# Performance work log

Hardware: AMD Instinct MI355X
Metric: run time of the kernel (lower is better)

## Reference

```python
import jax, jax.numpy as jnp
import numpy as np
import math

DIM = 1024
MLP = 4096
D_STATE = 16
D_CONV = 4
EXPAND = 2
D_INNER = EXPAND * DIM
HALF = D_INNER // 2
DT_RANK = math.ceil(DIM / 16)
BSZ = 2
SEQ = 2048
LN_EPS = 1e-5


def setup_inputs() -> dict:
    key = jax.random.key(0)
    ks = jax.random.split(key, 12)
    s = lambda k, shape, sc: jax.random.normal(k, shape, dtype=jnp.float32) * sc
    return {
        "x": s(ks[0], (BSZ, SEQ, DIM), 1.0),
        "ln1_g": jnp.ones((DIM,), jnp.float32),
        "ln1_b": jnp.zeros((DIM,), jnp.float32),
        "in_proj_w": s(ks[1], (D_INNER, DIM), 0.02),
        "conv_x_w": s(ks[2], (HALF, 1, D_CONV), 0.1),
        "conv_x_b": jnp.zeros((HALF,), jnp.float32),
        "conv_z_w": s(ks[3], (HALF, 1, D_CONV), 0.1),
        "conv_z_b": jnp.zeros((HALF,), jnp.float32),
        "x_proj_w": s(ks[4], (DT_RANK + 2 * D_STATE, HALF), 0.02),
        "dt_proj_w": s(ks[5], (HALF, DT_RANK), 0.02),
        "dt_proj_b": s(ks[6], (HALF,), 0.1),
        "A_log": jnp.log(jnp.tile(jnp.arange(1, D_STATE + 1, dtype=jnp.float32), (HALF, 1))),
        "Dp": jnp.ones((HALF,), jnp.float32),
        "out_proj_w": s(ks[7], (DIM, D_INNER), 0.02),
        "ln2_g": jnp.ones((DIM,), jnp.float32),
        "ln2_b": jnp.zeros((DIM,), jnp.float32),
        "mlp_w1": s(ks[8], (MLP, DIM), 0.02),
        "mlp_b1": jnp.zeros((MLP,), jnp.float32),
        "mlp_w2": s(ks[9], (DIM, MLP), 0.02),
        "mlp_b2": jnp.zeros((DIM,), jnp.float32),
    }


def _ln(x, g, b):
    mu = jnp.mean(x, -1, keepdims=True)
    v = jnp.mean((x - mu) ** 2, -1, keepdims=True)
    return (x - mu) * jax.lax.rsqrt(v + LN_EPS) * g + b


def _dwconv_same(x, w, b):
    # x: [B, C, L]; w: [C, 1, K] depthwise; PyTorch 'same' pads left=(K-1)//2, right=rest
    total = D_CONV - 1
    left = total // 2
    y = jax.lax.conv_general_dilated(
        x, w, (1,), [(left, total - left)],
        dimension_numbers=("NCH", "OIH", "NCH"),
        feature_group_count=x.shape[1])
    return y + b[None, :, None]


def _mixer(x, in_proj_w, conv_x_w, conv_x_b, conv_z_w, conv_z_b,
           x_proj_w, dt_proj_w, dt_proj_b, A_log, Dp, out_proj_w):
    Bsz = x.shape[0]
    xz = jnp.einsum('bld,ed->ble', x, in_proj_w)              # [B,L,2*HALF]
    xs, zs = jnp.split(xz, 2, axis=-1)
    xc = jax.nn.silu(_dwconv_same(jnp.swapaxes(xs, 1, 2), conv_x_w, conv_x_b))  # [B,HALF,L]
    zc = jax.nn.silu(_dwconv_same(jnp.swapaxes(zs, 1, 2), conv_z_w, conv_z_b))  # [B,HALF,L]
    u = jnp.swapaxes(xc, 1, 2)                                 # [B,L,HALF]
    x_dbl = jnp.einsum('bld,ed->ble', u, x_proj_w)             # [B,L,dt_rank+2N]
    dt, Bm, Cm = jnp.split(x_dbl, [DT_RANK, DT_RANK + D_STATE], axis=-1)
    delta = jax.nn.softplus(jnp.einsum('blr,dr->bld', dt, dt_proj_w) + dt_proj_b)  # [B,L,HALF]
    A = -jnp.exp(A_log)                                        # [HALF,N]
    dA = jnp.exp(jnp.einsum('bld,dn->lbdn', delta, A))         # [L,B,HALF,N]
    dBu = jnp.einsum('bld,bln,bld->lbdn', delta, Bm, u)        # [L,B,HALF,N]
    Cs = jnp.moveaxis(Cm, 1, 0)                                # [L,B,N]

    def step(h, t):
        dA_t, dBu_t, c_t = t
        h = dA_t * h + dBu_t                                   # [B,HALF,N]
        return h, jnp.einsum('bdn,bn->bd', h, c_t)

    h0 = jnp.zeros((Bsz, HALF, D_STATE), x.dtype)
    _, ys = jax.lax.scan(step, h0, (dA, dBu, Cs))              # ys: [L,B,HALF]
    y = jnp.moveaxis(ys, 0, 1) + u * Dp                        # [B,L,HALF]
    y = jnp.concatenate([y, jnp.swapaxes(zc, 1, 2)], axis=-1)  # [B,L,2*HALF]
    return jnp.einsum('ble,de->bld', y, out_proj_w)


def reference(x, ln1_g, ln1_b, in_proj_w, conv_x_w, conv_x_b, conv_z_w, conv_z_b,
              x_proj_w, dt_proj_w, dt_proj_b, A_log, Dp, out_proj_w,
              ln2_g, ln2_b, mlp_w1, mlp_b1, mlp_w2, mlp_b2):
    x = x + _mixer(_ln(x, ln1_g, ln1_b), in_proj_w, conv_x_w, conv_x_b,
                   conv_z_w, conv_z_b, x_proj_w, dt_proj_w, dt_proj_b,
                   A_log, Dp, out_proj_w)
    h = _ln(x, ln2_g, ln2_b)
    h = jax.nn.gelu(jnp.einsum('bld,md->blm', h, mlp_w1) + mlp_b1, approximate=False)
    h = jnp.einsum('blm,dm->bld', h, mlp_w2) + mlp_b2
    return x + h
```

## Files before the change

### kernel.cpp

```cpp
#include <hip/hip_runtime.h>
#include <math.h>

#define DIMD    1024
#define MLPD    4096
#define DSTATE  16
#define DCONV   4
#define HALF    1024
#define DINNER  2048
#define DTRANK  64
#define BSZ     2
#define SEQ     2048
#define NTOK    (BSZ*SEQ)
#define NCH     64
#define CL      (SEQ/NCH)

typedef short bf16x8 __attribute__((ext_vector_type(8)));
typedef float f32x4  __attribute__((ext_vector_type(4)));
typedef float f32x16 __attribute__((ext_vector_type(16)));
typedef unsigned short u16;
typedef unsigned int   u32;
typedef unsigned short u16x4 __attribute__((ext_vector_type(4)));

__device__ __forceinline__ u16 f2bf(float x) {
    union { float f; unsigned int u; } v; v.f = x;
    unsigned int r = (v.u + 0x7FFFu + ((v.u >> 16) & 1u)) >> 16;
    return (u16)r;
}
__device__ __forceinline__ float bf2f(u16 x) {
    union { unsigned int u; float f; } v; v.u = ((unsigned int)x) << 16;
    return v.f;
}

#define SZ_WIN  (DINNER*DIMD)
#define SZ_WXP  (96*HALF)
#define SZ_WDT  (HALF*DTRANK)
#define SZ_WOUT (DIMD*DINNER)
#define SZ_WM1  (MLPD*DIMD)
#define SZ_WM2  (DIMD*MLPD)
#define SZ_TOT  (SZ_WIN+SZ_WXP+SZ_WDT+SZ_WOUT+SZ_WM1+SZ_WM2)
#define CVT_BLOCKS (SZ_TOT / 1024)

__global__ __launch_bounds__(256) void cvtln_kernel(
        const float* __restrict__ x, const float* __restrict__ g,
        const float* __restrict__ b, u16* __restrict__ xn_bf,
        const float* __restrict__ s0, u16* __restrict__ d0,
        const float* __restrict__ s1, u16* __restrict__ d1,
        const float* __restrict__ s2, u16* __restrict__ d2,
        const float* __restrict__ s3, u16* __restrict__ d3,
        const float* __restrict__ s4, u16* __restrict__ d4,
        const float* __restrict__ s5, u16* __restrict__ d5) {
    if (blockIdx.x >= NTOK) {
        int i = (blockIdx.x - NTOK) * 1024 + threadIdx.x * 4;
        #define CVT4(s, d) { \
            float4 v = *(const float4*)((s) + i); \
            u16x4 o; o[0]=f2bf(v.x); o[1]=f2bf(v.y); o[2]=f2bf(v.z); o[3]=f2bf(v.w); \
            *(u16x4*)((d) + i) = o; }
        if (i < SZ_WIN)  { CVT4(s0, d0); return; }  i -= SZ_WIN;
        if (i < SZ_WXP)  { CVT4(s1, d1); return; }  i -= SZ_WXP;
        if (i < SZ_WDT)  { CVT4(s2, d2); return; }  i -= SZ_WDT;
        if (i < SZ_WOUT) { CVT4(s3, d3); return; }  i -= SZ_WOUT;
        if (i < SZ_WM1)  { CVT4(s4, d4); return; }  i -= SZ_WM1;
        if (i < SZ_WM2)  { CVT4(s5, d5); }
        #undef CVT4
        return;
    }
    __shared__ float sm[4];
    int row = blockIdx.x;
    int t = threadIdx.x;
    const float4* xr = (const float4*)(x + (size_t)row * DIMD);
    float4 v = xr[t];
    float s = v.x + v.y + v.z + v.w;
    for (int off = 32; off > 0; off >>= 1) s += __shfl_down(s, off, 64);
    if ((t & 63) == 0) sm[t >> 6] = s;
    __syncthreads();
    float mu = (sm[0] + sm[1] + sm[2] + sm[3]) * (1.0f / DIMD);
    float dx = v.x - mu, dy = v.y - mu, dz = v.z - mu, dw = v.w - mu;
    float ss = dx*dx + dy*dy + dz*dz + dw*dw;
    for (int off = 32; off > 0; off >>= 1) ss += __shfl_down(ss, off, 64);
    __syncthreads();
    if ((t & 63) == 0) sm[t >> 6] = ss;
    __syncthreads();
    float var = (sm[0] + sm[1] + sm[2] + sm[3]) * (1.0f / DIMD);
    float rs = rsqrtf(var + 1e-5f);
    float4 gv = ((const float4*)g)[t];
    float4 bv = ((const float4*)b)[t];
    u16* o = xn_bf + (size_t)row * DIMD + t * 4;
    o[0] = f2bf(dx * rs * gv.x + bv.x);
    o[1] = f2bf(dy * rs * gv.y + bv.y);
    o[2] = f2bf(dz * rs * gv.z + bv.z);
    o[3] = f2bf(dw * rs * gv.w + bv.w);
}

__global__ __launch_bounds__(256) void gemm_small_kernel(
        const u16* __restrict__ A, int lda,
        const u16* __restrict__ W, int K, int N,
        float* __restrict__ Cf, u16* __restrict__ Cb) {
    __shared__ f32x4 red[2][64];
    int t = threadIdx.x;
    int w = t >> 6, lane = t & 63;
    int mt = w & 1, kh = w >> 1;
    int m0 = blockIdx.x * 32 + mt * 16;
    int n0 = blockIdx.y * 16;
    int r = lane & 15, quad = lane >> 4;
    int Kh = K >> 1;
    f32x4 acc = {0.f, 0.f, 0.f, 0.f};
    const u16* ap = A + (size_t)(m0 + r) * lda + kh * Kh + quad * 8;
    const u16* wp = W + (size_t)(n0 + r) * K   + kh * Kh + quad * 8;
    for (int k = 0; k < Kh; k += 32) {
        bf16x8 av = *(const bf16x8*)(ap + k);
        bf16x8 bv = *(const bf16x8*)(wp + k);
        acc = __builtin_amdgcn_mfma_f32_16x16x32_bf16(av, bv, acc, 0, 0, 0);
    }
    if (kh == 1) red[mt][lane] = acc;
    __syncthreads();
    if (kh == 0) {
        f32x4 o = red[mt][lane];
        int col = n0 + r;
        #pragma unroll
        for (int i = 0; i < 4; ++i) {
            int row = m0 + quad * 4 + i;
            size_t idx = (size_t)row * N + col;
            float v = acc[i] + o[i];
            Cf[idx] = v;
            Cb[idx] = f2bf(v);
        }
    }
}

template<int EPI, int TN, int KS>
__global__ __launch_bounds__(256) void gemm128_kernel(
        const u16* __restrict__ A, int lda, const u16* __restrict__ W,
        int K, int N,
        const float* __restrict__ bias, const float* __restrict__ resid,
        float* __restrict__ Cf, float* __restrict__ Cf2,
        float* __restrict__ Cf3, float* __restrict__ Cf4,
        u16* __restrict__ Cb) {
    constexpr int NF = TN / 32;
    constexpr int NN = TN / 64;
    __shared__ u16 As0[128 * 32], As1[128 * 32];
    __shared__ u16 Bs0[TN * 32],  Bs1[TN * 32];
    const int t = threadIdx.x;
    const int w = t >> 6;
    const int lane = t & 63;
    const int r32 = lane & 31;
    const int kh  = lane >> 5;
    const int wm = w & 1, wn = w >> 1;
    const int m0 = blockIdx.x * 128;
    const int n0 = blockIdx.y * TN;
    const int Kloc = K / KS;
    const int kz = (KS > 1) ? blockIdx.z : 0;

    f32x16 acc[2][NN];
    #pragma unroll
    for (int mi = 0; mi < 2; ++mi)
        #pragma unroll
        for (int ni = 0; ni < NN; ++ni)
            acc[mi][ni] = (f32x16){0.f,0.f,0.f,0.f,0.f,0.f,0.f,0.f,
                                   0.f,0.f,0.f,0.f,0.f,0.f,0.f,0.f};

    const u16* pa[2];
    const u16* pb[NF / 2];
    #pragma unroll
    for (int i = 0; i < 2; ++i) {
        int c = (i * 4 + w) * 64 + lane;
        int row = c >> 2;
        int q = (c & 3) ^ ((row >> 1) & 3);
        pa[i] = A + (size_t)(m0 + row) * lda + (size_t)kz * Kloc + q * 8;
    }
    #pragma unroll
    for (int i = 0; i < NF / 2; ++i) {
        int c = (i * 4 + w) * 64 + lane;
        int row = c >> 2;
        int q = (c & 3) ^ ((row >> 1) & 3);
        pb[i] = W + (size_t)(n0 + row) * K + (size_t)kz * Kloc + q * 8;
    }
    const int gsw = (r32 >> 1) & 3;
    int aoff[2][2], boff[NN][2];
    #pragma unroll
    for (int mi = 0; mi < 2; ++mi)
        #pragma unroll
        for (int tt = 0; tt < 2; ++tt)
            aoff[mi][tt] = (wm * 64 + mi * 32 + r32) * 32 +
                           ((tt * 2 + kh) ^ gsw) * 8;
    #pragma unroll
    for (int ni = 0; ni < NN; ++ni)
        #pragma unroll
        for (int tt = 0; tt < 2; ++tt)
            boff[ni][tt] = (wn * (TN / 2) + ni * 32 + r32) * 32 +
                           ((tt * 2 + kh) ^ gsw) * 8;

    auto stage = [&](u16* __restrict__ Ad, u16* __restrict__ Bd) {
        #pragma unroll
        for (int i = 0; i < 2; ++i) {
            __builtin_amdgcn_global_load_lds(
                (const __attribute__((address_space(1))) u32*)pa[i],
                (__attribute__((address_space(3))) u32*)(Ad + (i * 4 + w) * 512),
                16, 0, 0);
            pa[i] += 32;
        }
        #pragma unroll
        for (int i = 0; i < NF / 2; ++i) {
            __builtin_amdgcn_global_load_lds(
                (const __attribute__((address_space(1))) u32*)pb[i],
                (__attribute__((address_space(3))) u32*)(Bd + (i * 4 + w) * 512),
                16, 0, 0);
            pb[i] += 32;
        }
    };
    auto compute = [&](const u16* __restrict__ Ab, const u16* __restrict__ Bb) {
        bf16x8 af[2][2], bfr[NN][2];
        #pragma unroll
        for (int mi = 0; mi < 2; ++mi)
            #pragma unroll
            for (int tt = 0; tt < 2; ++tt)
                af[mi][tt] = *(const bf16x8*)(Ab + aoff[mi][tt]);
        #pragma unroll
        for (int ni = 0; ni < NN; ++ni)
            #pragma unroll
            for (int tt = 0; tt < 2; ++tt)
                bfr[ni][tt] = *(const bf16x8*)(Bb + boff[ni][tt]);
        #pragma unroll
        for (int tt = 0; tt < 2; ++tt)
            #pragma unroll
            for (int mi = 0; mi < 2; ++mi)
                #pragma unroll
                for (int ni = 0; ni < NN; ++ni)
                    acc[mi][ni] = __builtin_amdgcn_mfma_f32_32x32x16_bf16(
                        af[mi][tt], bfr[ni][tt], acc[mi][ni], 0, 0, 0);
    };

    stage(As0, Bs0);
    for (int k0 = 0; k0 < Kloc; k0 += 64) {
        __syncthreads();
        if (k0 + 32 < Kloc) stage(As1, Bs1);
        compute(As0, Bs0);
        __syncthreads();
        if (k0 + 64 < Kloc) stage(As0, Bs0);
        compute(As1, Bs1);
    }

    float* Cfo = Cf;
    if (KS == 2 && kz == 1) Cfo = Cf2;
    if (KS == 4) Cfo = (kz == 0) ? Cf : (kz == 1) ? Cf2 : (kz == 2) ? Cf3 : Cf4;
    #pragma unroll
    for (int mi = 0; mi < 2; ++mi) {
        #pragma unroll
        for (int ni = 0; ni < NN; ++ni) {
            #pragma unroll
            for (int reg = 0; reg < 16; ++reg) {
                int row = m0 + wm * 64 + mi * 32 + (reg & 3) + 8 * (reg >> 2) + 4 * kh;
                int col = n0 + wn * (TN / 2) + ni * 32 + r32;
                size_t idx = (size_t)row * N + col;
                float v = acc[mi][ni][reg];
                if (EPI == 1) { v += bias[col]; v = (v > 20.f) ? v : log1pf(expf(v)); }
                if (EPI == 2) {
                    v += bias[col];
                    float e = __expf(fminf(1.5957691216f * v + 0.0713548162f * v * v * v, 80.f));
                    v = v * __fdividef(e, e + 1.f);
                }
                if (EPI == 3) { v += resid[idx]; }
                if (EPI == 4) { v += bias[col] + resid[idx]; }
                if (EPI == 2 || EPI == 5) Cb[idx] = f2bf(v);
                else                      Cfo[idx] = v;
            }
        }
    }
}

template<int EPI, int KS_>
__global__ __launch_bounds__(512) void gemm256_kernel(
        const u16* __restrict__ A, int lda, const u16* __restrict__ W,
        int K, int N,
        const float* __restrict__ bias,
        float* __restrict__ Cf, float* __restrict__ Cf2,
        float* __restrict__ Cf3, float* __restrict__ Cf4,
        u16* __restrict__ Cb) {
    __shared__ u16 As[2][256 * 64];
    __shared__ u16 Bs[2][256 * 64];
    const int t = threadIdx.x;
    const int lane = t & 63;
    const int w = t >> 6;
    const int r = lane & 15, q = lane >> 4;
    const int wm = w >> 2, wn = w & 3;
    const int m0 = blockIdx.x * 256;
    const int n0 = blockIdx.y * 256;
    const int kz = (KS_ > 1) ? blockIdx.z : 0;
    const int Kloc = K / KS_;
    const int NI = Kloc / 128;

    f32x4 acc[8][4];
    #pragma unroll
    for (int mi = 0; mi < 8; ++mi)
        #pragma unroll
        for (int ni = 0; ni < 4; ++ni)
            acc[mi][ni] = (f32x4){0.f, 0.f, 0.f, 0.f};

    const int aoffb = (wm * 128 + r) * 64;
    const int boffb = (wn * 64  + r) * 64;
    const int kswz[2] = { ((0 + q) ^ (r & 7)) * 8,
                          ((4 + q) ^ (r & 7)) * 8 };
    const int srow = t >> 3;
    const int scol = (((t & 7) ^ (srow & 7)) * 8);
    const int sdst = (t >> 6) * 512;
    const size_t kzoff = (size_t)kz * Kloc;

    auto stA = [&](int buf, int T, int j) {
        const u16* src = A + (size_t)(m0 + j * 64 + srow) * lda + kzoff + T * 64 + scol;
        __builtin_amdgcn_global_load_lds(
            (const __attribute__((address_space(1))) u32*)src,
            (__attribute__((address_space(3))) u32*)(&As[buf][j * 4096 + sdst]),
            16, 0, 0);
    };
    auto stB = [&](int buf, int T, int j) {
        const u16* src = W + (size_t)(n0 + j * 64 + srow) * (size_t)K + kzoff + T * 64 + scol;
        __builtin_amdgcn_global_load_lds(
            (const __attribute__((address_space(1))) u32*)src,
            (__attribute__((address_space(3))) u32*)(&Bs[buf][j * 4096 + sdst]),
            16, 0, 0);
    };

    bf16x8 bfr[4];

    #define PH(BUF, KSL, MH, STMT, VMODE)                                         \
    do {                                                                          \
        if (MH == 0) {                                                            \
            _Pragma("unroll")                                                     \
            for (int ni = 0; ni < 4; ++ni)                                        \
                bfr[ni] = *(const bf16x8*)(&Bs[BUF][boffb + ni * 1024 + kswz[KSL]]); \
        }                                                                         \
        bf16x8 af0 = *(const bf16x8*)(&As[BUF][aoffb + (MH*4+0)*1024 + kswz[KSL]]);  \
        bf16x8 af1 = *(const bf16x8*)(&As[BUF][aoffb + (MH*4+1)*1024 + kswz[KSL]]);  \
        bf16x8 af2 = *(const bf16x8*)(&As[BUF][aoffb + (MH*4+2)*1024 + kswz[KSL]]);  \
        bf16x8 af3 = *(const bf16x8*)(&As[BUF][aoffb + (MH*4+3)*1024 + kswz[KSL]]);  \
        STMT;                                                                     \
        VMODE;                                                                    \
        __builtin_amdgcn_s_barrier();                                             \
        asm volatile("s_waitcnt lgkmcnt(0)" ::: "memory");                        \
        __builtin_amdgcn_sched_barrier(0);                                        \
        __builtin_amdgcn_s_setprio(1);                                            \
        _Pragma("unroll")                                                         \
        for (int ni = 0; ni < 4; ++ni) {                                          \
            acc[MH*4+0][ni] = __builtin_amdgcn_mfma_f32_16x16x32_bf16(af0, bfr[ni], acc[MH*4+0][ni], 0, 0, 0); \
            acc[MH*4+1][ni] = __builtin_amdgcn_mfma_f32_16x16x32_bf16(af1, bfr[ni], acc[MH*4+1][ni], 0, 0, 0); \
            acc[MH*4+2][ni] = __builtin_amdgcn_mfma_f32_16x16x32_bf16(af2, bfr[ni], acc[MH*4+2][ni], 0, 0, 0); \
            acc[MH*4+3][ni] = __builtin_amdgcn_mfma_f32_16x16x32_bf16(af3, bfr[ni], acc[MH*4+3][ni], 0, 0, 0); \
        }                                                                         \
        __builtin_amdgcn_s_setprio(0);                                            \
        __builtin_amdgcn_s_barrier();                                             \
    } while (0)

    #define VM_NONE do {} while (0)
    #define VM_P3   do { if (more) asm volatile("s_waitcnt vmcnt(2)" ::: "memory"); \
                         else      asm volatile("s_waitcnt vmcnt(0)" ::: "memory"); } while (0)
    #define VM_P7   do { if (more) asm volatile("s_waitcnt vmcnt(2)" ::: "memory"); } while (0)

    #pragma unroll
    for (int j = 0; j < 4; ++j) stB(0, 0, j);
    #pragma unroll
    for (int j = 0; j < 4; ++j) stA(0, 0, j);
    stB(1, 1, 0); stB(1, 1, 1);
    asm volatile("s_waitcnt vmcnt(2)" ::: "memory");
    __builtin_amdgcn_s_barrier();

    for (int it = 0; it < NI; ++it) {
        const bool more = (it + 1) < NI;
        const int T1 = 2 * it + 1, T2 = T1 + 1, T3 = T1 + 2;
        PH(0, 0, 0, { stB(1, T1, 2); stB(1, T1, 3); }, VM_NONE);
        PH(0, 0, 1, { stA(1, T1, 0); stA(1, T1, 1); }, VM_NONE);
        PH(0, 1, 0, { stA(1, T1, 2); stA(1, T1, 3); }, VM_NONE);
        PH(0, 1, 1, { if (more) { stB(0, T2, 0); stB(0, T2, 1); } }, VM_P3);
        PH(1, 0, 0, { if (more) { stB(0, T2, 2); stB(0, T2, 3); } }, VM_NONE);
        PH(1, 0, 1, { if (more) { stA(0, T2, 0); stA(0, T2, 1); } }, VM_NONE);
        PH(1, 1, 0, { if (more) { stA(0, T2, 2); stA(0, T2, 3); } }, VM_NONE);
        PH(1, 1, 1, { if (more) { stB(1, T3, 0); stB(1, T3, 1); } }, VM_P7);
    }
    #undef PH
    #undef VM_NONE
    #undef VM_P3
    #undef VM_P7

    float* wsc = ((float*)&As[0][0]) + (size_t)w * (16 * 68);
    const int erow = lane >> 3;
    const int ecol = (lane & 7) * 4;
    float* Cfo = Cf;
    if (KS_ == 4) Cfo = (kz == 0) ? Cf : (kz == 1) ? Cf2 : (kz == 2) ? Cf3 : Cf4;
    #pragma unroll
    for (int mi = 0; mi < 8; ++mi) {
        #pragma unroll
        for (int ni = 0; ni < 4; ++ni)
            #pragma unroll
            for (int i = 0; i < 4; ++i)
                wsc[(q * 4 + i) * 68 + ni * 16 + r] = acc[mi][ni][i];
        asm volatile("s_waitcnt lgkmcnt(0)" ::: "memory");
        __builtin_amdgcn_sched_barrier(0);
        #pragma unroll
        for (int half = 0; half < 2; ++half) {
            #pragma unroll
            for (int k2 = 0; k2 < 2; ++k2) {
                int lr = half * 8 + erow;
                f32x4 v4 = *(const f32x4*)&wsc[lr * 68 + ecol + k2 * 32];
                int row = m0 + wm * 128 + mi * 16 + lr;
                int colb = n0 + wn * 64 + ecol + k2 * 32;
                size_t idx = (size_t)row * N + colb;
                if (EPI == 2) {
                    float4 bb = *(const float4*)&bias[colb];
                    float vv0 = v4[0] + bb.x, vv1 = v4[1] + bb.y;
                    float vv2 = v4[2] + bb.z, vv3 = v4[3] + bb.w;
                    u16x4 o;
                    #define GELU1(vx, slot) { \
                        float e = __expf(fminf(1.5957691216f * (vx) + 0.0713548162f * (vx)*(vx)*(vx), 80.f)); \
                        o[slot] = f2bf((vx) * __fdividef(e, e + 1.f)); }
                    GELU1(vv0, 0); GELU1(vv1, 1); GELU1(vv2, 2); GELU1(vv3, 3);
                    #undef GELU1
                    *(u16x4*)&Cb[idx] = o;
                } else {
                    *(f32x4*)&Cfo[idx] = v4;
                }
            }
        }
        asm volatile("s_waitcnt lgkmcnt(0)" ::: "memory");
        __builtin_amdgcn_sched_barrier(0);
    }
}

__global__ __launch_bounds__(256) void reduce4_kernel(
        const float* __restrict__ P0, const float* __restrict__ P1,
        const float* __restrict__ P2, const float* __restrict__ P3,
        const float* __restrict__ bias, const float* __restrict__ resid,
        float* __restrict__ out) {
    size_t idx = ((size_t)blockIdx.x * 256 + threadIdx.x) * 4;
    float4 a = *(const float4*)(P0 + idx);
    float4 b = *(const float4*)(P1 + idx);
    float4 c = *(const float4*)(P2 + idx);
    float4 d = *(const float4*)(P3 + idx);
    float4 rr = *(const float4*)(resid + idx);
    int col = (int)(idx & (DIMD - 1));
    float4 bb = *(const float4*)(bias + col);
    float4 o;
    o.x = a.x + b.x + c.x + d.x + rr.x + bb.x;
    o.y = a.y + b.y + c.y + d.y + rr.y + bb.y;
    o.z = a.z + b.z + c.z + d.z + rr.z + bb.z;
    o.w = a.w + b.w + c.w + d.w + rr.w + bb.w;
    *(float4*)(out + idx) = o;
}

__global__ __launch_bounds__(256) void reduce_ln4_kernel(
        const float* __restrict__ P0, const float* __restrict__ P1,
        const float* __restrict__ P2, const float* __restrict__ P3,
        const float* __restrict__ resid,
        const float* __restrict__ g, const float* __restrict__ b,
        float* __restrict__ x2, u16* __restrict__ out_bf) {
    __shared__ float sm[4];
    int row = blockIdx.x;
    int t = threadIdx.x;
    size_t base = (size_t)row * DIMD + t * 4;
    float4 a  = *(const float4*)(P0 + base);
    float4 p  = *(const float4*)(P1 + base);
    float4 c  = *(const float4*)(P2 + base);
    float4 d  = *(const float4*)(P3 + base);
    float4 rr = *(const float4*)(resid + base);
    float4 v;
    v.x = a.x + p.x + c.x + d.x + rr.x;
    v.y = a.y + p.y + c.y + d.y + rr.y;
    v.z = a.z + p.z + c.z + d.z + rr.z;
    v.w = a.w + p.w + c.w + d.w + rr.w;
    *(float4*)(x2 + base) = v;
    float s = v.x + v.y + v.z + v.w;
    for (int off = 32; off > 0; off >>= 1) s += __shfl_down(s, off, 64);
    if ((t & 63) == 0) sm[t >> 6] = s;
    __syncthreads();
    float mu = (sm[0] + sm[1] + sm[2] + sm[3]) * (1.0f / DIMD);
    float dx = v.x - mu, dy = v.y - mu, dz = v.z - mu, dw = v.w - mu;
    float ss = dx*dx + dy*dy + dz*dz + dw*dw;
    for (int off = 32; off > 0; off >>= 1) ss += __shfl_down(ss, off, 64);
    __syncthreads();
    if ((t & 63) == 0) sm[t >> 6] = ss;
    __syncthreads();
    float var = (sm[0] + sm[1] + sm[2] + sm[3]) * (1.0f / DIMD);
    float rs = rsqrtf(var + 1e-5f);
    float4 gv = ((const float4*)g)[t];
    float4 bv = ((const float4*)b)[t];
    u16* o = out_bf + base;
    o[0] = f2bf(dx * rs * gv.x + bv.x);
    o[1] = f2bf(dy * rs * gv.y + bv.y);
    o[2] = f2bf(dz * rs * gv.z + bv.z);
    o[3] = f2bf(dw * rs * gv.w + bv.w);
}

__global__ __launch_bounds__(256) void conv_silu_kernel(
        const u16* __restrict__ xz,
        const float* __restrict__ wx, const float* __restrict__ bx,
        const float* __restrict__ wz, const float* __restrict__ bz,
        u16* __restrict__ u_bf, u16* __restrict__ ycat) {
    int c  = blockIdx.x * 256 + threadIdx.x;
    int gy = blockIdx.y;
    int b  = gy >> 8;
    int l0 = (gy & 255) * 8;
    const u16* base = xz + ((size_t)(b * SEQ + l0)) * DINNER;
    float wxr[4], wzr[4];
    #pragma unroll
    for (int k = 0; k < 4; ++k) { wxr[k] = wx[c * 4 + k]; wzr[k] = wz[c * 4 + k]; }
    float bxv = bx[c], bzv = bz[c];
    float xm1 = (l0 > 0) ? bf2f(base[c - DINNER]) : 0.f;
    float x0v = bf2f(base[c]);
    float x1v = bf2f(base[c + DINNER]);
    float zm1 = (l0 > 0) ? bf2f(base[HALF + c - DINNER]) : 0.f;
    float z0v = bf2f(base[HALF + c]);
    float z1v = bf2f(base[HALF + c + DINNER]);
    u16* up = u_bf + ((size_t)(b * SEQ + l0)) * HALF + c;
    u16* yp = ycat + ((size_t)(b * SEQ + l0)) * DINNER + HALF + c;
    #pragma unroll
    for (int l = 0; l < 8; ++l) {
        bool in = (l0 + l + 2) < SEQ;
        float x2v = in ? bf2f(base[(size_t)(l + 2) * DINNER + c]) : 0.f;
        float z2v = in ? bf2f(base[(size_t)(l + 2) * DINNER + HALF + c]) : 0.f;
        float ax = bxv + wxr[0]*xm1 + wxr[1]*x0v + wxr[2]*x1v + wxr[3]*x2v;
        float az = bzv + wzr[0]*zm1 + wzr[1]*z0v + wzr[2]*z1v + wzr[3]*z2v;
        float sx = ax * __fdividef(1.f, 1.f + __expf(-ax));
        float sz = az * __fdividef(1.f, 1.f + __expf(-az));
        *up = f2bf(sx); *yp = f2bf(sz);
        up += HALF; yp += DINNER;
        xm1 = x0v; x0v = x1v; x1v = x2v;
        zm1 = z0v; z0v = z1v; z1v = z2v;
    }
}

__global__ __launch_bounds__(256) void scan_p1_kernel(
        const float* __restrict__ delta, const u16* __restrict__ u_bf,
        const float* __restrict__ x_dbl, const float* __restrict__ A_log,
        float* __restrict__ hfin, float* __restrict__ dsum) {
    int t  = blockIdx.x * 256 + threadIdx.x;
    int d  = t & (HALF - 1);
    int ch = (t >> 10) & (NCH - 1);
    int b  = t >> 16;
    float Ac[16], h[16];
    #pragma unroll
    for (int i = 0; i < 4; ++i) {
        float4 a = *(const float4*)&A_log[d * DSTATE + i * 4];
        Ac[4*i+0] = -__expf(a.x); Ac[4*i+1] = -__expf(a.y);
        Ac[4*i+2] = -__expf(a.z); Ac[4*i+3] = -__expf(a.w);
        h[4*i+0] = 0.f; h[4*i+1] = 0.f; h[4*i+2] = 0.f; h[4*i+3] = 0.f;
    }
    int l0 = b * SEQ + ch * CL;
    size_t off = (size_t)l0 * HALF + d;
    const float* xrow = x_dbl + (size_t)l0 * 96;
    float ds = 0.f;
    #pragma unroll 4
    for (int l = 0; l < CL; ++l) {
        float dl = delta[off];
        float uv = bf2f(u_bf[off]);
        off += HALF;
        float4 B0 = *(const float4*)(xrow + 64);
        float4 B1 = *(const float4*)(xrow + 68);
        float4 B2 = *(const float4*)(xrow + 72);
        float4 B3 = *(const float4*)(xrow + 76);
        xrow += 96;
        float dBu = dl * uv;
        ds += dl;
        float Bv[16] = {B0.x,B0.y,B0.z,B0.w, B1.x,B1.y,B1.z,B1.w,
                        B2.x,B2.y,B2.z,B2.w, B3.x,B3.y,B3.z,B3.w};
        #pragma unroll
        for (int n = 0; n < 16; ++n)
            h[n] = __expf(dl * Ac[n]) * h[n] + dBu * Bv[n];
    }
    float4* hf = (float4*)&hfin[(size_t)t * 16];
    #pragma unroll
    for (int i = 0; i < 4; ++i)
        hf[i] = (float4){h[4*i+0], h[4*i+1], h[4*i+2], h[4*i+3]};
    dsum[t] = ds;
}

__global__ __launch_bounds__(256) void scan_p2_kernel(
        const float* __restrict__ A_log, const float* __restrict__ dsum,
        const float* __restrict__ hfin, float* __restrict__ hin) {
    int t = blockIdx.x * 256 + threadIdx.x;
    int n = t & 15;
    int d = (t >> 4) & (HALF - 1);
    int b = t >> 14;
    float Ac = -__expf(A_log[d * DSTATE + n]);
    float h = 0.f;
    for (int ch = 0; ch < NCH; ++ch) {
        size_t chain = ((size_t)(b * NCH + ch) * HALF) + d;
        hin[chain * 16 + n] = h;
        float ds = dsum[chain];
        h = __expf(Ac * ds) * h + hfin[chain * 16 + n];
    }
}

__global__ __launch_bounds__(256) void scan_p3_kernel(
        const float* __restrict__ delta, const u16* __restrict__ u_bf,
        const float* __restrict__ x_dbl, const float* __restrict__ A_log,
        const float* __restrict__ Dp, const float* __restrict__ hin,
        u16* __restrict__ ycat) {
    int t  = blockIdx.x * 256 + threadIdx.x;
    int d  = t & (HALF - 1);
    int ch = (t >> 10) & (NCH - 1);
    int b  = t >> 16;
    float Ac[16], h[16];
    #pragma unroll
    for (int i = 0; i < 4; ++i) {
        float4 a  = *(const float4*)&A_log[d * DSTATE + i * 4];
        float4 hv = *(const float4*)&hin[(size_t)t * 16 + i * 4];
        Ac[4*i+0] = -__expf(a.x); Ac[4*i+1] = -__expf(a.y);
        Ac[4*i+2] = -__expf(a.z); Ac[4*i+3] = -__expf(a.w);
        h[4*i+0] = hv.x; h[4*i+1] = hv.y; h[4*i+2] = hv.z; h[4*i+3] = hv.w;
    }
    float Dv = Dp[d];
    int l0 = b * SEQ + ch * CL;
    size_t off = (size_t)l0 * HALF + d;
    const float* xrow = x_dbl + (size_t)l0 * 96;
    u16* yp = ycat + (size_t)l0 * DINNER + d;
    #pragma unroll 4
    for (int l = 0; l < CL; ++l) {
        float dl = delta[off];
        float uv = bf2f(u_bf[off]);
        off += HALF;
        float4 B0 = *(const float4*)(xrow + 64);
        float4 B1 = *(const float4*)(xrow + 68);
        float4 B2 = *(const float4*)(xrow + 72);
        float4 B3 = *(const float4*)(xrow + 76);
        float4 C0 = *(const float4*)(xrow + 80);
        float4 C1 = *(const float4*)(xrow + 84);
        float4 C2 = *(const float4*)(xrow + 88);
        float4 C3 = *(const float4*)(xrow + 92);
        xrow += 96;
        float dBu = dl * uv;
        float Bv[16] = {B0.x,B0.y,B0.z,B0.w, B1.x,B1.y,B1.z,B1.w,
                        B2.x,B2.y,B2.z,B2.w, B3.x,B3.y,B3.z,B3.w};
        float Cv[16] = {C0.x,C0.y,C0.z,C0.w, C1.x,C1.y,C1.z,C1.w,
                        C2.x,C2.y,C2.z,C2.w, C3.x,C3.y,C3.z,C3.w};
        float y = uv * Dv;
        #pragma unroll
        for (int n = 0; n < 16; ++n) {
            h[n] = __expf(dl * Ac[n]) * h[n] + dBu * Bv[n];
            y += h[n] * Cv[n];
        }
        *yp = f2bf(y);
        yp += DINNER;
    }
}

extern "C" void kernel_launch(void* const* d_in, const int* in_sizes, int n_in,
                              void* d_out, int out_size, void* d_ws, size_t ws_size,
                              hipStream_t stream) {
    const float* x         = (const float*)d_in[0];
    const float* ln1_g     = (const float*)d_in[1];
    const float* ln1_b     = (const float*)d_in[2];
    const float* in_proj_w = (const float*)d_in[3];
    const float* conv_x_w  = (const float*)d_in[4];
    const float* conv_x_b  = (const float*)d_in[5];
    const float* conv_z_w  = (const float*)d_in[6];
    const float* conv_z_b  = (const float*)d_in[7];
    const float* x_proj_w  = (const float*)d_in[8];
    const float* dt_proj_w = (const float*)d_in[9];
    const float* dt_proj_b = (const float*)d_in[10];
    const float* A_log     = (const float*)d_in[11];
    const float* Dp        = (const float*)d_in[12];
    const float* out_proj_w= (const float*)d_in[13];
    const float* ln2_g     = (const float*)d_in[14];
    const float* ln2_b     = (const float*)d_in[15];
    const float* mlp_w1    = (const float*)d_in[16];
    const float* mlp_b1    = (const float*)d_in[17];
    const float* mlp_w2    = (const float*)d_in[18];
    const float* mlp_b2    = (const float*)d_in[19];
    float* out = (float*)d_out;

    char* p = (char*)d_ws;
    auto alloc = [&](size_t bytes) {
        char* r = p; p += (bytes + 255) & ~(size_t)255; return r;
    };
    const size_t MB16 = (size_t)16 * 1024 * 1024;
    u16*   w_in   = (u16*)  alloc((size_t)DINNER * DIMD * 2);
    u16*   w_xp   = (u16*)  alloc((size_t)96 * HALF * 2);
    u16*   w_dt   = (u16*)  alloc((size_t)HALF * DTRANK * 2);
    u16*   w_out  = (u16*)  alloc((size_t)DIMD * DINNER * 2);
    u16*   w_m1   = (u16*)  alloc((size_t)MLPD * DIMD * 2);
    u16*   w_m2   = (u16*)  alloc((size_t)DIMD * MLPD * 2);
    char*  Pb     =         alloc(4 * MB16);
    float* delta  = (float*)(Pb);
    u16*   xz_bf  = (u16*)  (Pb + 1 * MB16);
    u16*   ycat   = (u16*)  (Pb + 2 * MB16);
    u16*   u_bf   = (u16*)  (Pb + 3 * MB16);
    u16*   xn_bf  = (u16*)  (Pb + 3 * MB16 + MB16 / 2);
    float* x_dbl  = (float*)alloc((size_t)NTOK * 96 * 4);
    u16*   xdbl_bf= (u16*)  alloc((size_t)NTOK * 96 * 2);
    float* x2     = (float*)alloc((size_t)NTOK * DIMD * 4);
    u16*   ln2_bf = (u16*)  alloc((size_t)NTOK * DIMD * 2);
    u16*   mlp_h  = (u16*)  alloc((size_t)NTOK * MLPD * 2);
    float* hfin = (float*)mlp_h;
    float* hin  = hfin + (size_t)BSZ * NCH * HALF * DSTATE;
    float* dsum = hin  + (size_t)BSZ * NCH * HALF * DSTATE;
    float* R0 = (float*)(Pb);
    float* R1 = (float*)(Pb + 1 * MB16);
    float* R2 = (float*)mlp_h;
    float* R3 = (float*)((char*)mlp_h + MB16);
    float* Q0 = (float*)(Pb);
    float* Q1 = (float*)(Pb + 1 * MB16);
    float* Q2 = (float*)(Pb + 2 * MB16);
    float* Q3 = (float*)(Pb + 3 * MB16);

    cvtln_kernel<<<NTOK + CVT_BLOCKS, 256, 0, stream>>>(
        x, ln1_g, ln1_b, xn_bf,
        in_proj_w, w_in, x_proj_w, w_xp, dt_proj_w, w_dt,
        out_proj_w, w_out, mlp_w1, w_m1, mlp_w2, w_m2);

    gemm128_kernel<5,128,1><<<dim3(NTOK/128, DINNER/128), 256, 0, stream>>>(
        xn_bf, DIMD, w_in, DIMD, DINNER, nullptr, nullptr,
        nullptr, nullptr, nullptr, nullptr, xz_bf);

    conv_silu_kernel<<<dim3(HALF/256, NTOK/8), 256, 0, stream>>>(
        xz_bf, conv_x_w, conv_x_b, conv_z_w, conv_z_b, u_bf, ycat);

    gemm_small_kernel<<<dim3(NTOK/32, 96/16), 256, 0, stream>>>(
        u_bf, HALF, w_xp, HALF, 96, x_dbl, xdbl_bf);

    gemm128_kernel<1,64,1><<<dim3(NTOK/128, HALF/64), 256, 0, stream>>>(
        xdbl_bf, 96, w_dt, DTRANK, HALF, dt_proj_b, nullptr,
        delta, nullptr, nullptr, nullptr, nullptr);

    scan_p1_kernel<<<(BSZ*NCH*HALF)/256, 256, 0, stream>>>(
        delta, u_bf, x_dbl, A_log, hfin, dsum);
    scan_p2_kernel<<<(BSZ*HALF*DSTATE)/256, 256, 0, stream>>>(
        A_log, dsum, hfin, hin);
    scan_p3_kernel<<<(BSZ*NCH*HALF)/256, 256, 0, stream>>>(
        delta, u_bf, x_dbl, A_log, Dp, hin, ycat);

    gemm256_kernel<0,4><<<dim3(NTOK/256, DIMD/256, 4), 512, 0, stream>>>(
        ycat, DINNER, w_out, DINNER, DIMD, nullptr,
        R0, R1, R2, R3, nullptr);
    reduce_ln4_kernel<<<NTOK, 256, 0, stream>>>(
        R0, R1, R2, R3, x, ln2_g, ln2_b, x2, ln2_bf);

    gemm256_kernel<2,1><<<dim3(NTOK/256, MLPD/256, 1), 512, 0, stream>>>(
        ln2_bf, DIMD, w_m1, DIMD, MLPD, mlp_b1,
        nullptr, nullptr, nullptr, nullptr, mlp_h);

    gemm256_kernel<0,4><<<dim3(NTOK/256, DIMD/256, 4), 512, 0, stream>>>(
        mlp_h, MLPD, w_m2, MLPD, DIMD, nullptr,
        Q0, Q1, Q2, Q3, nullptr);
    reduce4_kernel<<<(NTOK*DIMD)/1024, 256, 0, stream>>>(
        Q0, Q1, Q2, Q3, mlp_b2, x2, out);
}
```

Baseline: 415.4 us.

## Replace split-K partial buffers and reduce kernels with atomic accumulation into residual

The split-K GEMMs for out_proj and mlp_w2 now add their partial tiles directly into the residual buffers with float atomics. Before, each split wrote a separate partial buffer and a reduce kernel summed the four. The residual x is copied into x2 during the first LN kernel, and the LN2 kernel pre-writes x2 plus mlp_b2 into the output so the final GEMM can accumulate onto it. This drops two full partial-buffer write/read passes and one kernel launch. In exchange it adds scalar atomic traffic and nondeterministic summation order, and the workspace is no longer aliased, so it uses more memory.

```diff
diff --git a/kernel.cpp b/kernel.cpp
--- a/kernel.cpp
+++ b/kernel.cpp
@@ -43,6 +43,7 @@
 __global__ __launch_bounds__(256) void cvtln_kernel(
         const float* __restrict__ x, const float* __restrict__ g,
         const float* __restrict__ b, u16* __restrict__ xn_bf,
+        float* __restrict__ x2,
         const float* __restrict__ s0, u16* __restrict__ d0,
         const float* __restrict__ s1, u16* __restrict__ d1,
         const float* __restrict__ s2, u16* __restrict__ d2,
@@ -67,8 +68,10 @@
     __shared__ float sm[4];
     int row = blockIdx.x;
     int t = threadIdx.x;
+    size_t base = (size_t)row * DIMD + t * 4;
     const float4* xr = (const float4*)(x + (size_t)row * DIMD);
     float4 v = xr[t];
+    *(float4*)(x2 + base) = v;
     float s = v.x + v.y + v.z + v.w;
     for (int off = 32; off > 0; off >>= 1) s += __shfl_down(s, off, 64);
     if ((t & 63) == 0) sm[t >> 6] = s;
@@ -84,7 +87,7 @@
     float rs = rsqrtf(var + 1e-5f);
     float4 gv = ((const float4*)g)[t];
     float4 bv = ((const float4*)b)[t];
-    u16* o = xn_bf + (size_t)row * DIMD + t * 4;
+    u16* o = xn_bf + base;
     o[0] = f2bf(dx * rs * gv.x + bv.x);
     o[1] = f2bf(dy * rs * gv.y + bv.y);
     o[2] = f2bf(dz * rs * gv.z + bv.z);
@@ -383,7 +386,8 @@
     const int erow = lane >> 3;
     const int ecol = (lane & 7) * 4;
     float* Cfo = Cf;
-    if (KS_ == 4) Cfo = (kz == 0) ? Cf : (kz == 1) ? Cf2 : (kz == 2) ? Cf3 : Cf4;
+    if (EPI == 0 && KS_ == 4)
+        Cfo = (kz == 0) ? Cf : (kz == 1) ? Cf2 : (kz == 2) ? Cf3 : Cf4;
     #pragma unroll
     for (int mi = 0; mi < 8; ++mi) {
         #pragma unroll
@@ -413,6 +417,11 @@
                     GELU1(vv0, 0); GELU1(vv1, 1); GELU1(vv2, 2); GELU1(vv3, 3);
                     #undef GELU1
                     *(u16x4*)&Cb[idx] = o;
+                } else if (EPI == 6) {
+                    atomicAdd(&Cf[idx + 0], v4[0]);
+                    atomicAdd(&Cf[idx + 1], v4[1]);
+                    atomicAdd(&Cf[idx + 2], v4[2]);
+                    atomicAdd(&Cf[idx + 3], v4[3]);
                 } else {
                     *(f32x4*)&Cfo[idx] = v4;
                 }
@@ -423,48 +432,21 @@
     }
 }
 
-__global__ __launch_bounds__(256) void reduce4_kernel(
-        const float* __restrict__ P0, const float* __restrict__ P1,
-        const float* __restrict__ P2, const float* __restrict__ P3,
-        const float* __restrict__ bias, const float* __restrict__ resid,
-        float* __restrict__ out) {
-    size_t idx = ((size_t)blockIdx.x * 256 + threadIdx.x) * 4;
-    float4 a = *(const float4*)(P0 + idx);
-    float4 b = *(const float4*)(P1 + idx);
-    float4 c = *(const float4*)(P2 + idx);
-    float4 d = *(const float4*)(P3 + idx);
-    float4 rr = *(const float4*)(resid + idx);
-    int col = (int)(idx & (DIMD - 1));
-    float4 bb = *(const float4*)(bias + col);
-    float4 o;
-    o.x = a.x + b.x + c.x + d.x + rr.x + bb.x;
-    o.y = a.y + b.y + c.y + d.y + rr.y + bb.y;
-    o.z = a.z + b.z + c.z + d.z + rr.z + bb.z;
-    o.w = a.w + b.w + c.w + d.w + rr.w + bb.w;
-    *(float4*)(out + idx) = o;
-}
-
-__global__ __launch_bounds__(256) void reduce_ln4_kernel(
-        const float* __restrict__ P0, const float* __restrict__ P1,
-        const float* __restrict__ P2, const float* __restrict__ P3,
-        const float* __restrict__ resid,
+__global__ __launch_bounds__(256) void ln_kernel(
+        const float* __restrict__ x2,
         const float* __restrict__ g, const float* __restrict__ b,
-        float* __restrict__ x2, u16* __restrict__ out_bf) {
+        const float* __restrict__ b2,
+        u16* __restrict__ out_bf, float* __restrict__ outpre) {
     __shared__ float sm[4];
     int row = blockIdx.x;
     int t = threadIdx.x;
     size_t base = (size_t)row * DIMD + t * 4;
-    float4 a  = *(const float4*)(P0 + base);
-    float4 p  = *(const float4*)(P1 + base);
-    float4 c  = *(const float4*)(P2 + base);
-    float4 d  = *(const float4*)(P3 + base);
-    float4 rr = *(const float4*)(resid + base);
-    float4 v;
-    v.x = a.x + p.x + c.x + d.x + rr.x;
-    v.y = a.y + p.y + c.y + d.y + rr.y;
-    v.z = a.z + p.z + c.z + d.z + rr.z;
-    v.w = a.w + p.w + c.w + d.w + rr.w;
-    *(float4*)(x2 + base) = v;
+    float4 v = *(const float4*)(x2 + base);
+    float4 b2v = ((const float4*)b2)[t];
+    float4 op;
+    op.x = v.x + b2v.x; op.y = v.y + b2v.y;
+    op.z = v.z + b2v.z; op.w = v.w + b2v.w;
+    *(float4*)(outpre + base) = op;
     float s = v.x + v.y + v.z + v.w;
     for (int off = 32; off > 0; off >>= 1) s += __shfl_down(s, off, 64);
     if ((t & 63) == 0) sm[t >> 6] = s;
@@ -669,38 +651,28 @@
     auto alloc = [&](size_t bytes) {
         char* r = p; p += (bytes + 255) & ~(size_t)255; return r;
     };
-    const size_t MB16 = (size_t)16 * 1024 * 1024;
     u16*   w_in   = (u16*)  alloc((size_t)DINNER * DIMD * 2);
     u16*   w_xp   = (u16*)  alloc((size_t)96 * HALF * 2);
     u16*   w_dt   = (u16*)  alloc((size_t)HALF * DTRANK * 2);
     u16*   w_out  = (u16*)  alloc((size_t)DIMD * DINNER * 2);
     u16*   w_m1   = (u16*)  alloc((size_t)MLPD * DIMD * 2);
     u16*   w_m2   = (u16*)  alloc((size_t)DIMD * MLPD * 2);
-    char*  Pb     =         alloc(4 * MB16);
-    float* delta  = (float*)(Pb);
-    u16*   xz_bf  = (u16*)  (Pb + 1 * MB16);
-    u16*   ycat   = (u16*)  (Pb + 2 * MB16);
-    u16*   u_bf   = (u16*)  (Pb + 3 * MB16);
-    u16*   xn_bf  = (u16*)  (Pb + 3 * MB16 + MB16 / 2);
+    u16*   xn_bf  = (u16*)  alloc((size_t)NTOK * DIMD * 2);
+    u16*   xz_bf  = (u16*)  alloc((size_t)NTOK * DINNER * 2);
+    u16*   u_bf   = (u16*)  alloc((size_t)NTOK * HALF * 2);
+    u16*   ycat   = (u16*)  alloc((size_t)NTOK * DINNER * 2);
     float* x_dbl  = (float*)alloc((size_t)NTOK * 96 * 4);
     u16*   xdbl_bf= (u16*)  alloc((size_t)NTOK * 96 * 2);
+    float* delta  = (float*)alloc((size_t)NTOK * HALF * 4);
     float* x2     = (float*)alloc((size_t)NTOK * DIMD * 4);
     u16*   ln2_bf = (u16*)  alloc((size_t)NTOK * DIMD * 2);
     u16*   mlp_h  = (u16*)  alloc((size_t)NTOK * MLPD * 2);
     float* hfin = (float*)mlp_h;
     float* hin  = hfin + (size_t)BSZ * NCH * HALF * DSTATE;
     float* dsum = hin  + (size_t)BSZ * NCH * HALF * DSTATE;
-    float* R0 = (float*)(Pb);
-    float* R1 = (float*)(Pb + 1 * MB16);
-    float* R2 = (float*)mlp_h;
-    float* R3 = (float*)((char*)mlp_h + MB16);
-    float* Q0 = (float*)(Pb);
-    float* Q1 = (float*)(Pb + 1 * MB16);
-    float* Q2 = (float*)(Pb + 2 * MB16);
-    float* Q3 = (float*)(Pb + 3 * MB16);
 
     cvtln_kernel<<<NTOK + CVT_BLOCKS, 256, 0, stream>>>(
-        x, ln1_g, ln1_b, xn_bf,
+        x, ln1_g, ln1_b, xn_bf, x2,
         in_proj_w, w_in, x_proj_w, w_xp, dt_proj_w, w_dt,
         out_proj_w, w_out, mlp_w1, w_m1, mlp_w2, w_m2);
 
@@ -725,19 +697,18 @@
     scan_p3_kernel<<<(BSZ*NCH*HALF)/256, 256, 0, stream>>>(
         delta, u_bf, x_dbl, A_log, Dp, hin, ycat);
 
-    gemm256_kernel<0,4><<<dim3(NTOK/256, DIMD/256, 4), 512, 0, stream>>>(
+    gemm256_kernel<6,4><<<dim3(NTOK/256, DIMD/256, 4), 512, 0, stream>>>(
         ycat, DINNER, w_out, DINNER, DIMD, nullptr,
-        R0, R1, R2, R3, nullptr);
-    reduce_ln4_kernel<<<NTOK, 256, 0, stream>>>(
-        R0, R1, R2, R3, x, ln2_g, ln2_b, x2, ln2_bf);
+        x2, nullptr, nullptr, nullptr, nullptr);
+
+    ln_kernel<<<NTOK, 256, 0, stream>>>(
+        x2, ln2_g, ln2_b, mlp_b2, ln2_bf, out);
 
     gemm256_kernel<2,1><<<dim3(NTOK/256, MLPD/256, 1), 512, 0, stream>>>(
         ln2_bf, DIMD, w_m1, DIMD, MLPD, mlp_b1,
         nullptr, nullptr, nullptr, nullptr, mlp_h);
 
-    gemm256_kernel<0,4><<<dim3(NTOK/256, DIMD/256, 4), 512, 0, stream>>>(
+    gemm256_kernel<6,4><<<dim3(NTOK/256, DIMD/256, 4), 512, 0, stream>>>(
         mlp_h, MLPD, w_m2, MLPD, DIMD, nullptr,
-        Q0, Q1, Q2, Q3, nullptr);
-    reduce4_kernel<<<(NTOK*DIMD)/1024, 256, 0, stream>>>(
-        Q0, Q1, Q2, Q3, mlp_b2, x2, out);
-}
+        out, nullptr, nullptr, nullptr, nullptr);
+}
```

Result: slower. 780.2 us (+87.8%).

## Restructure 256x256 GEMM into four-stage K=32 LDS ring pipeline

Applied to the files above, without the earlier changes.

Replaces the double-buffered K=64 tiles in the 256x256 GEMM with a 4-slot ring of K=32 half-tiles. Loads run three stages ahead, and the vmcnt waits are adjusted so each barrier waits only for the oldest stage. The LDS swizzle changes to suit 32-wide rows. The aim is deeper prefetch to hide global-load latency, at the cost of twice as many barriers per unit of K and a new swizzle that may raise bank conflicts.

```diff
diff --git a/kernel.cpp b/kernel.cpp
--- a/kernel.cpp
+++ b/kernel.cpp
@@ -275,8 +275,8 @@
         float* __restrict__ Cf, float* __restrict__ Cf2,
         float* __restrict__ Cf3, float* __restrict__ Cf4,
         u16* __restrict__ Cb) {
-    __shared__ u16 As[2][256 * 64];
-    __shared__ u16 Bs[2][256 * 64];
+    __shared__ u16 AH[4][256 * 32];
+    __shared__ u16 BH[4][256 * 32];
     const int t = threadIdx.x;
     const int lane = t & 63;
     const int w = t >> 6;
@@ -286,7 +286,7 @@
     const int n0 = blockIdx.y * 256;
     const int kz = (KS_ > 1) ? blockIdx.z : 0;
     const int Kloc = K / KS_;
-    const int NI = Kloc / 128;
+    const int NH = Kloc / 32;
 
     f32x4 acc[8][4];
     #pragma unroll
@@ -295,43 +295,42 @@
         for (int ni = 0; ni < 4; ++ni)
             acc[mi][ni] = (f32x4){0.f, 0.f, 0.f, 0.f};
 
-    const int aoffb = (wm * 128 + r) * 64;
-    const int boffb = (wn * 64  + r) * 64;
-    const int kswz[2] = { ((0 + q) ^ (r & 7)) * 8,
-                          ((4 + q) ^ (r & 7)) * 8 };
-    const int srow = t >> 3;
-    const int scol = (((t & 7) ^ (srow & 7)) * 8);
-    const int sdst = (t >> 6) * 512;
+    const int gsw  = (q ^ (r & 3)) * 8;
+    const int abase = (wm * 128 + r) * 32 + gsw;
+    const int bbase = (wn * 64  + r) * 32 + gsw;
+    const int srow = t >> 2;
+    const int scol = (((t & 3) ^ ((t >> 2) & 3)) * 8);
+    const int sdst = w * 512;
     const size_t kzoff = (size_t)kz * Kloc;
 
-    auto stA = [&](int buf, int T, int j) {
-        const u16* src = A + (size_t)(m0 + j * 64 + srow) * lda + kzoff + T * 64 + scol;
+    auto stA = [&](int buf, int s, int j) {
+        const u16* src = A + (size_t)(m0 + j * 128 + srow) * lda + kzoff + s * 32 + scol;
         __builtin_amdgcn_global_load_lds(
             (const __attribute__((address_space(1))) u32*)src,
-            (__attribute__((address_space(3))) u32*)(&As[buf][j * 4096 + sdst]),
+            (__attribute__((address_space(3))) u32*)(&AH[buf][j * 4096 + sdst]),
             16, 0, 0);
     };
-    auto stB = [&](int buf, int T, int j) {
-        const u16* src = W + (size_t)(n0 + j * 64 + srow) * (size_t)K + kzoff + T * 64 + scol;
+    auto stB = [&](int buf, int s, int j) {
+        const u16* src = W + (size_t)(n0 + j * 128 + srow) * (size_t)K + kzoff + s * 32 + scol;
         __builtin_amdgcn_global_load_lds(
             (const __attribute__((address_space(1))) u32*)src,
-            (__attribute__((address_space(3))) u32*)(&Bs[buf][j * 4096 + sdst]),
+            (__attribute__((address_space(3))) u32*)(&BH[buf][j * 4096 + sdst]),
             16, 0, 0);
     };
 
     bf16x8 bfr[4];
 
-    #define PH(BUF, KSL, MH, STMT, VMODE)                                         \
+    #define PH(BUF, MH, STMT, VMODE)                                              \
     do {                                                                          \
         if (MH == 0) {                                                            \
             _Pragma("unroll")                                                     \
             for (int ni = 0; ni < 4; ++ni)                                        \
-                bfr[ni] = *(const bf16x8*)(&Bs[BUF][boffb + ni * 1024 + kswz[KSL]]); \
+                bfr[ni] = *(const bf16x8*)(&BH[BUF][bbase + ni * 512]);           \
         }                                                                         \
-        bf16x8 af0 = *(const bf16x8*)(&As[BUF][aoffb + (MH*4+0)*1024 + kswz[KSL]]);  \
-        bf16x8 af1 = *(const bf16x8*)(&As[BUF][aoffb + (MH*4+1)*1024 + kswz[KSL]]);  \
-        bf16x8 af2 = *(const bf16x8*)(&As[BUF][aoffb + (MH*4+2)*1024 + kswz[KSL]]);  \
-        bf16x8 af3 = *(const bf16x8*)(&As[BUF][aoffb + (MH*4+3)*1024 + kswz[KSL]]);  \
+        bf16x8 af0 = *(const bf16x8*)(&AH[BUF][abase + (MH*4+0)*512]);            \
+        bf16x8 af1 = *(const bf16x8*)(&AH[BUF][abase + (MH*4+1)*512]);            \
+        bf16x8 af2 = *(const bf16x8*)(&AH[BUF][abase + (MH*4+2)*512]);            \
+        bf16x8 af3 = *(const bf16x8*)(&AH[BUF][abase + (MH*4+3)*512]);            \
         STMT;                                                                     \
         VMODE;                                                                    \
         __builtin_amdgcn_s_barrier();                                             \
@@ -350,40 +349,38 @@
     } while (0)
 
     #define VM_NONE do {} while (0)
-    #define VM_P3   do { if (more) asm volatile("s_waitcnt vmcnt(2)" ::: "memory"); \
-                         else      asm volatile("s_waitcnt vmcnt(0)" ::: "memory"); } while (0)
-    #define VM_P7   do { if (more) asm volatile("s_waitcnt vmcnt(2)" ::: "memory"); } while (0)
-
-    #pragma unroll
-    for (int j = 0; j < 4; ++j) stB(0, 0, j);
-    #pragma unroll
-    for (int j = 0; j < 4; ++j) stA(0, 0, j);
-    stB(1, 1, 0); stB(1, 1, 1);
-    asm volatile("s_waitcnt vmcnt(2)" ::: "memory");
+    #define VM_TAIL do {                                                          \
+        if (st)               asm volatile("s_waitcnt vmcnt(8)" ::: "memory");    \
+        else if (s + 2 < NH)  asm volatile("s_waitcnt vmcnt(4)" ::: "memory");    \
+        else if (s + 1 < NH)  asm volatile("s_waitcnt vmcnt(0)" ::: "memory");    \
+    } while (0)
+
+    #pragma unroll
+    for (int h = 0; h < 3; ++h) {
+        stA(h, h, 0); stA(h, h, 1);
+        stB(h, h, 0); stB(h, h, 1);
+    }
+    asm volatile("s_waitcnt vmcnt(8)" ::: "memory");
     __builtin_amdgcn_s_barrier();
 
-    for (int it = 0; it < NI; ++it) {
-        const bool more = (it + 1) < NI;
-        const int T1 = 2 * it + 1, T2 = T1 + 1, T3 = T1 + 2;
-        PH(0, 0, 0, { stB(1, T1, 2); stB(1, T1, 3); }, VM_NONE);
-        PH(0, 0, 1, { stA(1, T1, 0); stA(1, T1, 1); }, VM_NONE);
-        PH(0, 1, 0, { stA(1, T1, 2); stA(1, T1, 3); }, VM_NONE);
-        PH(0, 1, 1, { if (more) { stB(0, T2, 0); stB(0, T2, 1); } }, VM_P3);
-        PH(1, 0, 0, { if (more) { stB(0, T2, 2); stB(0, T2, 3); } }, VM_NONE);
-        PH(1, 0, 1, { if (more) { stA(0, T2, 0); stA(0, T2, 1); } }, VM_NONE);
-        PH(1, 1, 0, { if (more) { stA(0, T2, 2); stA(0, T2, 3); } }, VM_NONE);
-        PH(1, 1, 1, { if (more) { stB(1, T3, 0); stB(1, T3, 1); } }, VM_P7);
+    for (int s = 0; s < NH; ++s) {
+        const int  b  = s & 3;
+        const int  s3 = s + 3;
+        const int  b3 = s3 & 3;
+        const bool st = s3 < NH;
+        PH(b, 0, { if (st) { stA(b3, s3, 0); stA(b3, s3, 1); } }, VM_NONE);
+        PH(b, 1, { if (st) { stB(b3, s3, 0); stB(b3, s3, 1); } }, VM_TAIL);
     }
     #undef PH
     #undef VM_NONE
-    #undef VM_P3
-    #undef VM_P7
-
-    float* wsc = ((float*)&As[0][0]) + (size_t)w * (16 * 68);
+    #undef VM_TAIL
+
+    float* wsc = ((float*)&AH[0][0]) + (size_t)w * (16 * 68);
     const int erow = lane >> 3;
     const int ecol = (lane & 7) * 4;
     float* Cfo = Cf;
-    if (KS_ == 4) Cfo = (kz == 0) ? Cf : (kz == 1) ? Cf2 : (kz == 2) ? Cf3 : Cf4;
+    if (KS_ == 4)
+        Cfo = (kz == 0) ? Cf : (kz == 1) ? Cf2 : (kz == 2) ? Cf3 : Cf4;
     #pragma unroll
     for (int mi = 0; mi < 8; ++mi) {
         #pragma unroll
```

After: 423.2 us. No clear change (+1.9%).
